# Performance work log

Hardware: AMD Instinct MI355X
Metric: run time of the kernel (lower is better)

Reference implementation:

```python
import jax, jax.numpy as jnp
import numpy as np

B, TT, T, L, V, E, H = 16, 8, 64, 100, 32000, 512, 512
EO = 2 * H          # encoder output size == decoder hidden size
A = 512             # attention size
IN = E + EO + E     # decoder raw input size
TEMP = IN // 2      # sharp_linear output size
sg = jax.lax.stop_gradient


def _lstm_cell(x, h, c, Wih, Whh, bih, bhh):
    # PyTorch LSTM gate order: i, f, g, o
    g = x @ Wih.T + bih + h @ Whh.T + bhh
    i, f, gg, o = jnp.split(g, 4, axis=-1)
    c = jax.nn.sigmoid(f) * c + jax.nn.sigmoid(i) * jnp.tanh(gg)
    h = jax.nn.sigmoid(o) * jnp.tanh(c)
    return h, c


def setup_inputs():
    key = jax.random.key(0)
    ks = jax.random.split(key, 24)
    s = 0.05
    rn = lambda k, sh: jax.random.normal(k, sh, jnp.float32) * s
    z = lambda *sh: jnp.zeros(sh, jnp.float32)
    return {
        "embedding": rn(ks[0], (V, E)),
        "enc_Wih_f": rn(ks[1], (4 * H, E)), "enc_Whh_f": rn(ks[2], (4 * H, H)),
        "enc_bih_f": z(4 * H), "enc_bhh_f": z(4 * H),
        "enc_Wih_b": rn(ks[3], (4 * H, E)), "enc_Whh_b": rn(ks[4], (4 * H, H)),
        "enc_bih_b": z(4 * H), "enc_bhh_b": z(4 * H),
        "W1": rn(ks[5], (A, EO)), "W2": rn(ks[6], (A, EO)),
        "mem_W": rn(ks[7], (E, EO)), "mem_b": z(E),
        "U1": rn(ks[8], (E, E)), "V1": rn(ks[9], (E, E)),
        "U2": rn(ks[10], (E, E)), "V2": rn(ks[11], (E, E)),
        "sharp_W": rn(ks[12], (TEMP, IN)), "sharp_b": z(TEMP),
        "dec_Wih": rn(ks[13], (4 * EO, TEMP)), "dec_Whh": rn(ks[14], (4 * EO, EO)),
        "dec_bih": z(4 * EO), "dec_bhh": z(4 * EO),
        "fc_W": rn(ks[15], (V, EO)), "fc_b": z(V),
        "topic": jax.random.randint(ks[16], (B, TT), 0, V),
        "topic_len": jnp.full((B,), TT, jnp.int32),
        "essay_input": jax.random.randint(ks[17], (B, T), 0, V),
        "essay_len": jnp.full((B,), T, jnp.int32),
        "mems": jax.random.randint(ks[18], (B, L), 0, V),
    }


def reference(embedding, enc_Wih_f, enc_Whh_f, enc_bih_f, enc_bhh_f,
              enc_Wih_b, enc_Whh_b, enc_bih_b, enc_bhh_b,
              W1, W2, mem_W, mem_b, U1, V1, U2, V2,
              sharp_W, sharp_b, dec_Wih, dec_Whh, dec_bih, dec_bhh,
              fc_W, fc_b, topic, topic_len, essay_input, essay_len, mems):
    Bsz = topic.shape[0]
    Tlen = essay_input.shape[1]

    # ---------------- Encoder (1-layer bidirectional LSTM) ----------------
    # all topic_len equal -> pack/sort is identity
    x = embedding[topic].transpose(1, 0, 2)  # [TT, B, E]

    def mk_cell(Wih, Whh, bih, bhh):
        def f(carry, xt):
            h, c = carry
            h, c = _lstm_cell(xt, h, c, Wih, Whh, bih, bhh)
            return (h, c), h
        return f

    z0 = (jnp.zeros((Bsz, H), x.dtype), jnp.zeros((Bsz, H), x.dtype))
    (hf, cf), outs_f = jax.lax.scan(mk_cell(enc_Wih_f, enc_Whh_f, enc_bih_f, enc_bhh_f), z0, x)
    (hb, cb), outs_b = jax.lax.scan(mk_cell(enc_Wih_b, enc_Whh_b, enc_bih_b, enc_bhh_b), z0, x[::-1])
    outs_b = outs_b[::-1]
    topics = jnp.concatenate([outs_f, outs_b], axis=-1).transpose(1, 0, 2)  # [B, TT, 2H]
    h = jnp.concatenate([hf, hb], axis=-1)  # [B, EO]
    c = jnp.concatenate([cf, cb], axis=-1)  # [B, EO]

    # ---------------- external memory ----------------
    M = embedding[mems]                      # [B, L, E]
    pre_t = topics @ W1.T                    # [B, TT, A]  (precompute attention keys)

    def update_memory(M, emb):
        # all reads of stored memory are detached in the original module
        Md = sg(M)
        e = emb[:, None, :]                  # [B, 1, E]
        Mt = jnp.tanh(Md @ U1.T + e @ V1.T)
        gate = jax.nn.sigmoid(Md @ U2.T + e @ V2.T)
        Mn = gate * Mt + (1.0 - gate) * Md
        return jnp.where(jnp.isfinite(Mn), Mn, jnp.float32(1e-31))

    def before_feed(emb, h_last, c_last, M):
        # topic attention (query = decoder cell state)
        q = c_last @ W2.T                                       # [B, A]
        alpha = jax.nn.softmax(jnp.einsum('bta,ba->bt', pre_t, q), axis=1)
        c_t = jnp.einsum('btd,bt->bd', topics, alpha)           # [B, EO]
        # content-addressed memory read (query = decoder hidden)
        v = jnp.tanh(h_last @ mem_W.T + mem_b)                  # [B, E]
        Md = sg(M)
        qm = jax.nn.softmax(jnp.einsum('ble,be->bl', Md, v), axis=1)
        m_t = jnp.einsum('bl,ble->be', qm, Md)                  # [B, E]
        return jnp.concatenate([emb, c_t, m_t], axis=1)         # [B, IN]

    # ---------------- decode (teacher forcing) ----------------
    emb0 = embedding[essay_input[:, 0]]
    M = update_memory(M, emb0)
    dec_in = before_feed(emb0, h, c, M)

    # steps 1..T-1 feed essay_input[:, t]; last scan step's memory update is unused
    toks = jnp.concatenate([essay_input[:, 1:], essay_input[:, -1:]], axis=1).T  # [T, B]

    def step(carry, tok):
        h, c, M, dec_in = carry
        xs = dec_in @ sharp_W.T + sharp_b
        h, c = _lstm_cell(xs, h, c, dec_Wih, dec_Whh, dec_bih, dec_bhh)
        logits = h @ fc_W.T + fc_b                              # [B, V]
        emb = embedding[tok]
        M = update_memory(M, emb)
        dec_in = before_feed(emb, h, c, M)
        return (h, c, M, dec_in), logits

    _, logits = jax.lax.scan(step, (h, c, M, dec_in), toks)
    return logits.transpose(1, 0, 2)  # [B, T, V]
```

## Files before the change

kernel.cpp:

```cpp
#include <hip/hip_runtime.h>
#include <math.h>

#define DEVI __device__ __forceinline__

typedef unsigned short us8 __attribute__((ext_vector_type(8)));
typedef short bfv __attribute__((ext_vector_type(8)));
typedef float f32x4 __attribute__((ext_vector_type(4)));

DEVI float sigmf_(float x){ return 1.0f/(1.0f+expf(-x)); }
DEVI float dot4_(const float4 a, const float4 b){ return a.x*b.x + a.y*b.y + a.z*b.z + a.w*b.w; }
DEVI float wred64(float v){
#pragma unroll
  for (int m = 32; m; m >>= 1) v += __shfl_xor(v, m);
  return v;
}
DEVI float b2f(unsigned short u){ return __uint_as_float(((unsigned)u)<<16); }
DEVI unsigned short f2bf(float x){
  unsigned u = __float_as_uint(x);
  return (unsigned short)((u + 0x7FFFu + ((u>>16)&1u)) >> 16);
}
DEVI void f2bf2(float x, unsigned short& hi, unsigned short& lo){
  hi = f2bf(x);
  lo = f2bf(x - b2f(hi));
}
DEVI unsigned short f2bf_lo(float x, unsigned short hi){
  return f2bf(x - b2f(hi));
}

DEVI float dotg(const unsigned short* wb, const float4* xr, int i8, float acc){
  us8 w = ((const us8*)wb)[i8];
  float4 xa = xr[2*i8], xb = xr[2*i8+1];
  acc += b2f(w[0])*xa.x; acc += b2f(w[1])*xa.y; acc += b2f(w[2])*xa.z; acc += b2f(w[3])*xa.w;
  acc += b2f(w[4])*xb.x; acc += b2f(w[5])*xb.y; acc += b2f(w[6])*xb.z; acc += b2f(w[7])*xb.w;
  return acc;
}
DEVI float dotg(const float* wb, const float4* xr, int i8, float acc){
  float4 wa = ((const float4*)wb)[2*i8], wv = ((const float4*)wb)[2*i8+1];
  float4 xa = xr[2*i8], xb = xr[2*i8+1];
  acc += wa.x*xa.x; acc += wa.y*xa.y; acc += wa.z*xa.z; acc += wa.w*xa.w;
  acc += wv.x*xb.x; acc += wv.y*xb.y; acc += wv.z*xb.z; acc += wv.w*xb.w;
  return acc;
}
template<typename WT>
DEVI float kdot1024(const WT* wbase, const float4* xr){
  float a0=0,a1=0,a2=0,a3=0;
#pragma unroll 4
  for (int it = 0; it < 32; ++it){
    a0 = dotg(wbase, xr, it*4+0, a0);
    a1 = dotg(wbase, xr, it*4+1, a1);
    a2 = dotg(wbase, xr, it*4+2, a2);
    a3 = dotg(wbase, xr, it*4+3, a3);
  }
  return (a0+a1)+(a2+a3);
}


__global__ void zero2_k(float* __restrict__ a, float* __restrict__ b, int n){
  int i = blockIdx.x*256 + threadIdx.x;
  if (i < n){ a[i] = 0.f; b[i] = 0.f; }
}

__global__ void gather_k(const float* __restrict__ emb, const int* __restrict__ topic,
                         const int* __restrict__ essay, const int* __restrict__ mems,
                         float* __restrict__ xtop, float* __restrict__ embs,
                         float* __restrict__ Mraw,
                         unsigned short* __restrict__ Mhi, unsigned short* __restrict__ Mlo)
{
  int r = blockIdx.x, tid = threadIdx.x;
  int idx; float* dst; size_t boff = 0; bool wb = false;
  if (r < 128){ int tt = r>>4, b = r&15; idx = topic[b*8+tt]; dst = xtop + (size_t)r*512; }
  else if (r < 1168){ int rr = r-128; int s = rr>>4, b = rr&15; int col = s < 64 ? s : 63;
                      idx = essay[b*64+col]; dst = embs + (size_t)rr*512; }
  else { int rr = r-1168; idx = mems[rr]; dst = Mraw + (size_t)rr*512;
         boff = (size_t)rr*512; wb = (Mhi != nullptr); }
  const float4* s4 = (const float4*)(emb + (size_t)idx*512);
  float4 v = s4[tid];
  ((float4*)dst)[tid] = v;
  if (wb){
    ushort4 h, l;
    f2bf2(v.x, h.x, l.x); f2bf2(v.y, h.y, l.y);
    f2bf2(v.z, h.z, l.z); f2bf2(v.w, h.w, l.w);
    ((ushort4*)(Mhi+boff))[tid] = h;
    ((ushort4*)(Mlo+boff))[tid] = l;
  }
}

__global__ void pack_k(const float* __restrict__ U1, const float* __restrict__ U2,
                       const float* __restrict__ sharpW,
                       float* __restrict__ UcatI, float* __restrict__ Ws3T)
{
  int gid = blockIdx.x*256 + threadIdx.x;
  if (gid < 524288){
    int n = gid>>9, k = gid&511;
    UcatI[gid] = (n&1) ? U2[(size_t)(n>>1)*512+k] : U1[(size_t)(n>>1)*512+k];
  } else {
    int g2 = gid - 524288;
    int k = g2>>10, j = g2&1023;
    Ws3T[g2] = sharpW[(size_t)j*2048 + 1536 + k];
  }
}

__global__ void pack_u_hilo(const float* __restrict__ U1, const float* __restrict__ U2,
                            unsigned short* __restrict__ Uhi, unsigned short* __restrict__ Ulo)
{
  int gid = blockIdx.x*256 + threadIdx.x;
  int n = gid>>9, k = gid&511;
  float v = (n&1) ? U2[(size_t)(n>>1)*512+k] : U1[(size_t)(n>>1)*512+k];
  unsigned short h, l;
  f2bf2(v, h, l);
  Uhi[gid] = h; Ulo[gid] = l;
}

__global__ void pack_ws3b(const float* __restrict__ sharpW,
                          unsigned short* __restrict__ hi, unsigned short* __restrict__ lo)
{
  int gid = blockIdx.x*256 + threadIdx.x;
  int j = gid>>9, k = gid&511;
  float v = sharpW[(size_t)j*2048 + 1536 + k];
  unsigned short h, l;
  f2bf2(v, h, l);
  hi[gid] = h; lo[gid] = l;
}

__global__ void conv_k(const float* __restrict__ src, unsigned short* __restrict__ dst, int n8){
  int i = blockIdx.x*256 + threadIdx.x;
  if (i >= n8) return;
  float4 a = ((const float4*)src)[2*i], b = ((const float4*)src)[2*i+1];
  us8 o;
  o[0]=f2bf(a.x); o[1]=f2bf(a.y); o[2]=f2bf(a.z); o[3]=f2bf(a.w);
  o[4]=f2bf(b.x); o[5]=f2bf(b.y); o[6]=f2bf(b.z); o[7]=f2bf(b.w);
  ((us8*)dst)[i] = o;
}

__global__ void conv2_k(const float* __restrict__ src,
                        unsigned short* __restrict__ hi, unsigned short* __restrict__ lo, int n8){
  int i = blockIdx.x*256 + threadIdx.x;
  if (i >= n8) return;
  float4 a = ((const float4*)src)[2*i], b = ((const float4*)src)[2*i+1];
  us8 oh, ol;
  oh[0]=f2bf(a.x); ol[0]=f2bf_lo(a.x, oh[0]);
  oh[1]=f2bf(a.y); ol[1]=f2bf_lo(a.y, oh[1]);
  oh[2]=f2bf(a.z); ol[2]=f2bf_lo(a.z, oh[2]);
  oh[3]=f2bf(a.w); ol[3]=f2bf_lo(a.w, oh[3]);
  oh[4]=f2bf(b.x); ol[4]=f2bf_lo(b.x, oh[4]);
  oh[5]=f2bf(b.y); ol[5]=f2bf_lo(b.y, oh[5]);
  oh[6]=f2bf(b.z); ol[6]=f2bf_lo(b.z, oh[6]);
  oh[7]=f2bf(b.w); ol[7]=f2bf_lo(b.w, oh[7]);
  ((us8*)hi)[i] = oh;
  ((us8*)lo)[i] = ol;
}

template<int ACT>
__global__ void gemm_nt(const float* __restrict__ A, int lda,
                        const float* __restrict__ W, int ldw, int woff,
                        const float* __restrict__ bias,
                        float* __restrict__ C, int ldc, int M, int N, int K)
{
  __shared__ float As[1024], Ws[1024];
  const int bm = blockIdx.y*64, bn = blockIdx.x*64;
  const int tid = threadIdx.x;
  const int lr = tid>>2, lk = (tid&3)<<2;
  const int tm = (tid>>4)<<2, tn = (tid&15)<<2;
  float acc[4][4] = {};
  for (int k0 = 0; k0 < K; k0 += 16){
    float4 av = make_float4(0.f,0.f,0.f,0.f);
    if (bm+lr < M) av = *(const float4*)(A + (size_t)(bm+lr)*lda + k0 + lk);
    As[(lk+0)*64+lr]=av.x; As[(lk+1)*64+lr]=av.y; As[(lk+2)*64+lr]=av.z; As[(lk+3)*64+lr]=av.w;
    float4 wv = make_float4(0.f,0.f,0.f,0.f);
    if (bn+lr < N) wv = *(const float4*)(W + (size_t)(bn+lr)*ldw + woff + k0 + lk);
    Ws[(lk+0)*64+lr]=wv.x; Ws[(lk+1)*64+lr]=wv.y; Ws[(lk+2)*64+lr]=wv.z; Ws[(lk+3)*64+lr]=wv.w;
    __syncthreads();
#pragma unroll
    for (int k = 0; k < 16; ++k){
      float4 a = *(const float4*)&As[k*64+tm];
      float4 w = *(const float4*)&Ws[k*64+tn];
      acc[0][0]+=a.x*w.x; acc[0][1]+=a.x*w.y; acc[0][2]+=a.x*w.z; acc[0][3]+=a.x*w.w;
      acc[1][0]+=a.y*w.x; acc[1][1]+=a.y*w.y; acc[1][2]+=a.y*w.z; acc[1][3]+=a.y*w.w;
      acc[2][0]+=a.z*w.x; acc[2][1]+=a.z*w.y; acc[2][2]+=a.z*w.z; acc[2][3]+=a.z*w.w;
      acc[3][0]+=a.w*w.x; acc[3][1]+=a.w*w.y; acc[3][2]+=a.w*w.z; acc[3][3]+=a.w*w.w;
    }
    __syncthreads();
  }
#pragma unroll
  for (int i = 0; i < 4; ++i){
    int m = bm+tm+i; if (m >= M) continue;
#pragma unroll
    for (int j = 0; j < 4; ++j){
      int n = bn+tn+j; if (n >= N) continue;
      float v = acc[i][j] + (bias ? bias[n] : 0.f);
      if (ACT == 1) v = tanhf(v);
      C[(size_t)m*ldc + n] = v;
    }
  }
}

__global__ void enc_step(const float* __restrict__ xtop,
    const float* __restrict__ Wih_f, const float* __restrict__ Whh_f,
    const float* __restrict__ bih_f, const float* __restrict__ bhh_f,
    const float* __restrict__ Wih_b, const float* __restrict__ Whh_b,
    const float* __restrict__ bih_b, const float* __restrict__ bhh_b,
    const float* __restrict__ h_in, const float* __restrict__ c_in,
    float* __restrict__ h_out, float* __restrict__ c_out,
    float* __restrict__ topics, int t)
{
  const int dir = blockIdx.y;
  const int j = blockIdx.x*4 + (threadIdx.x>>6);
  const int lane = threadIdx.x & 63;
  const int b = lane & 15, g4 = lane >> 4;
  const int tt = dir ? (7 - t) : t;
  const float* Wih = dir ? Wih_b : Wih_f;
  const float* Whh = dir ? Whh_b : Whh_f;
  const float* bih = dir ? bih_b : bih_f;
  const float* bhh = dir ? bhh_b : bhh_f;
  const int row = g4*512 + j;
  float acc = bih[row] + bhh[row];
  const float4* wx = (const float4*)(Wih + (size_t)row*512);
  const float4* xv = (const float4*)(xtop + (size_t)(tt*16+b)*512);
#pragma unroll 8
  for (int k = 0; k < 128; ++k) acc += dot4_(wx[k], xv[k]);
  const float4* wh = (const float4*)(Whh + (size_t)row*512);
  const float4* hv = (const float4*)(h_in + (size_t)b*1024 + dir*512);
#pragma unroll 8
  for (int k = 0; k < 128; ++k) acc += dot4_(wh[k], hv[k]);
  float gi = __shfl(acc, b);
  float gf = __shfl(acc, b+16);
  float gg = __shfl(acc, b+32);
  float go = __shfl(acc, b+48);
  if (g4 == 0){
    float c_old = c_in[(size_t)b*1024 + dir*512 + j];
    float cn = sigmf_(gf)*c_old + sigmf_(gi)*tanhf(gg);
    float hn = sigmf_(go)*tanhf(cn);
    h_out[(size_t)b*1024 + dir*512 + j] = hn;
    c_out[(size_t)b*1024 + dir*512 + j] = cn;
    topics[(size_t)(b*8+tt)*1024 + dir*512 + j] = hn;
  }
}

DEVI void mem_gemm_role(int bid, const float* __restrict__ Min, float* __restrict__ Mout,
                        const float* __restrict__ U,
                        const float* __restrict__ eV1s, const float* __restrict__ eV2s,
                        float* lds, int tid)
{
  const int bm = (bid>>4)*64, bn = (bid&15)*64;
  float* As = lds; float* Ws = lds + 1024;
  const int lr = tid>>2, lk = (tid&3)<<2;
  const int tm = (tid>>4)<<2, tn = (tid&15)<<2;
  float acc[4][4] = {};
  for (int k0 = 0; k0 < 512; k0 += 16){
    float4 av = *(const float4*)(Min + (size_t)(bm+lr)*512 + k0 + lk);
    As[(lk+0)*64+lr]=av.x; As[(lk+1)*64+lr]=av.y; As[(lk+2)*64+lr]=av.z; As[(lk+3)*64+lr]=av.w;
    float4 wv = *(const float4*)(U + (size_t)(bn+lr)*512 + k0 + lk);
    Ws[(lk+0)*64+lr]=wv.x; Ws[(lk+1)*64+lr]=wv.y; Ws[(lk+2)*64+lr]=wv.z; Ws[(lk+3)*64+lr]=wv.w;
    __syncthreads();
#pragma unroll
    for (int k = 0; k < 16; ++k){
      float4 a = *(const float4*)&As[k*64+tm];
      float4 w = *(const float4*)&Ws[k*64+tn];
      acc[0][0]+=a.x*w.x; acc[0][1]+=a.x*w.y; acc[0][2]+=a.x*w.z; acc[0][3]+=a.x*w.w;
      acc[1][0]+=a.y*w.x; acc[1][1]+=a.y*w.y; acc[1][2]+=a.y*w.z; acc[1][3]+=a.y*w.w;
      acc[2][0]+=a.z*w.x; acc[2][1]+=a.z*w.y; acc[2][2]+=a.z*w.z; acc[2][3]+=a.z*w.w;
      acc[3][0]+=a.w*w.x; acc[3][1]+=a.w*w.y; acc[3][2]+=a.w*w.z; acc[3][3]+=a.w*w.w;
    }
    __syncthreads();
  }
  const int e0 = (bn+tn)>>1;
#pragma unroll
  for (int i = 0; i < 4; ++i){
    int r = bm+tm+i;
    int b = r/100;
#pragma unroll
    for (int p = 0; p < 2; ++p){
      int e = e0 + p;
      float oldv = Min[(size_t)r*512 + e];
      float mt = tanhf (acc[i][2*p]   + eV1s[(size_t)b*512 + e]);
      float g  = sigmf_(acc[i][2*p+1] + eV2s[(size_t)b*512 + e]);
      float mn = g*mt + (1.f-g)*oldv;
      if (!isfinite(mn)) mn = 1e-31f;
      Mout[(size_t)r*512 + e] = mn;
    }
  }
}

__global__ void mem_update_k(const float* __restrict__ Min, float* __restrict__ Mout,
                             const float* __restrict__ U,
                             const float* __restrict__ eV1s, const float* __restrict__ eV2s)
{
  __shared__ float lds[2080];
  mem_gemm_role(blockIdx.x, Min, Mout, U, eV1s, eV2s, lds, threadIdx.x);
}

DEVI void mem_ep(f32x4 v, int m0, int n0, int i, int j, int kg, int r16, int lane,
                 const float* __restrict__ Min,
                 const float* __restrict__ eV1s, const float* __restrict__ eV2s,
                 float* __restrict__ Mout,
                 unsigned short* __restrict__ Mohi, unsigned short* __restrict__ Molo)
{
#pragma unroll
  for (int q = 0; q < 4; ++q){
    float val = v[q];
    float oth = __shfl_xor(val, 1);
    if (!(lane&1)){
      int m = m0 + i*16 + kg*4 + q;
      int n = n0 + j*16 + r16;
      int e = n>>1, bb = m/100;
      float mold = Min[(size_t)m*512 + e];
      float mt = tanhf (val + eV1s[(size_t)bb*512 + e]);
      float g  = sigmf_(oth + eV2s[(size_t)bb*512 + e]);
      float mn = g*mt + (1.f-g)*mold;
      if (!isfinite(mn)) mn = 1e-31f;
      Mout[(size_t)m*512 + e] = mn;
      unsigned short h, l;
      f2bf2(mn, h, l);
      Mohi[(size_t)m*512 + e] = h;
      Molo[(size_t)m*512 + e] = l;
    }
  }
}

DEVI void mem_mfma_role2(int hwbid, const float* __restrict__ Min,
                        const unsigned short* __restrict__ Mhi, const unsigned short* __restrict__ Mlo,
                        float* __restrict__ Mout,
                        unsigned short* __restrict__ Mohi, unsigned short* __restrict__ Molo,
                        const unsigned short* __restrict__ Uhi, const unsigned short* __restrict__ Ulo,
                        const float* __restrict__ eV1s, const float* __restrict__ eV2s,
                        int tid, float* __restrict__ lds)
{
  const int bid2 = (hwbid & 7)*200 + (hwbid >> 3);
  const int bm = (bid2 >> 5)*32, bn = (bid2 & 31)*32;
  const int wave = tid>>6, lane = tid&63;
  const int r16 = lane&15, kg = lane>>4;
  const size_t aoff = (size_t)(bm + r16)*512 + wave*128 + kg*8;
  const size_t boff = (size_t)(bn + r16)*512 + wave*128 + kg*8;
  const unsigned short* pa0h = Mhi + aoff; const unsigned short* pa0l = Mlo + aoff;
  const unsigned short* pb0h = Uhi + boff; const unsigned short* pb0l = Ulo + boff;
  f32x4 c00 = {}, c01 = {}, c10 = {}, c11 = {};
#pragma unroll
  for (int k0 = 0; k0 < 128; k0 += 32){
    bfv a0h = *(const bfv*)(pa0h + k0);
    bfv a0l = *(const bfv*)(pa0l + k0);
    bfv a1h = *(const bfv*)(pa0h + 16*512 + k0);
    bfv a1l = *(const bfv*)(pa0l + 16*512 + k0);
    bfv b0h = *(const bfv*)(pb0h + k0);
    bfv b0l = *(const bfv*)(pb0l + k0);
    bfv b1h = *(const bfv*)(pb0h + 16*512 + k0);
    bfv b1l = *(const bfv*)(pb0l + 16*512 + k0);
    c00 = __builtin_amdgcn_mfma_f32_16x16x32_bf16(a0h, b0h, c00, 0, 0, 0);
    c00 = __builtin_amdgcn_mfma_f32_16x16x32_bf16(a0h, b0l, c00, 0, 0, 0);
    c00 = __builtin_amdgcn_mfma_f32_16x16x32_bf16(a0l, b0h, c00, 0, 0, 0);
    c01 = __builtin_amdgcn_mfma_f32_16x16x32_bf16(a0h, b1h, c01, 0, 0, 0);
    c01 = __builtin_amdgcn_mfma_f32_16x16x32_bf16(a0h, b1l, c01, 0, 0, 0);
    c01 = __builtin_amdgcn_mfma_f32_16x16x32_bf16(a0l, b1h, c01, 0, 0, 0);
    c10 = __builtin_amdgcn_mfma_f32_16x16x32_bf16(a1h, b0h, c10, 0, 0, 0);
    c10 = __builtin_amdgcn_mfma_f32_16x16x32_bf16(a1h, b0l, c10, 0, 0, 0);
    c10 = __builtin_amdgcn_mfma_f32_16x16x32_bf16(a1l, b0h, c10, 0, 0, 0);
    c11 = __builtin_amdgcn_mfma_f32_16x16x32_bf16(a1h, b1h, c11, 0, 0, 0);
    c11 = __builtin_amdgcn_mfma_f32_16x16x32_bf16(a1h, b1l, c11, 0, 0, 0);
    c11 = __builtin_amdgcn_mfma_f32_16x16x32_bf16(a1l, b1h, c11, 0, 0, 0);
  }
  float* wbase = lds + wave*1024 + lane*4;
#pragma unroll
  for (int q = 0; q < 4; ++q){
    wbase[q]     = c00[q];
    wbase[256+q] = c01[q];
    wbase[512+q] = c10[q];
    wbase[768+q] = c11[q];
  }
  __syncthreads();
  f32x4 s;
#pragma unroll
  for (int q = 0; q < 4; ++q)
    s[q] = lds[       wave*256 + lane*4 + q] + lds[1024 + wave*256 + lane*4 + q]
         + lds[2048 + wave*256 + lane*4 + q] + lds[3072 + wave*256 + lane*4 + q];
  mem_ep(s, bm, bn, wave>>1, wave&1, kg, r16, lane, Min, eV1s, eV2s, Mout, Mohi, Molo);
}

__global__ __launch_bounds__(256,4) void mem_update_k2(
    const float* __restrict__ Min,
    const unsigned short* __restrict__ Mhi, const unsigned short* __restrict__ Mlo,
    float* __restrict__ Mout,
    unsigned short* __restrict__ Mohi, unsigned short* __restrict__ Molo,
    const unsigned short* __restrict__ Uhi, const unsigned short* __restrict__ Ulo,
    const float* __restrict__ eV1s, const float* __restrict__ eV2s)
{
  __shared__ float lds[4096];
  mem_mfma_role2(blockIdx.x, Min, Mhi, Mlo, Mout, Mohi, Molo, Uhi, Ulo, eV1s, eV2s, threadIdx.x, lds);
}

DEVI void logits_role(int lb, int tid,
    const unsigned short* __restrict__ fcWb, const float* __restrict__ fcb,
    const unsigned short* __restrict__ hh, const unsigned short* __restrict__ hl,
    float* __restrict__ out, int t)
{
  const int wave = tid>>6, lane = tid&63;
  const int r16 = lane&15, kg = lane>>4;
  const int tile = lb*4 + wave;
  const unsigned short* pa0 = fcWb + (size_t)(tile*16 + r16)*1024 + kg*8;
  const unsigned short* pbh = hh + (size_t)r16*1024 + kg*8;
  const unsigned short* pbl = hl + (size_t)r16*1024 + kg*8;
  f32x4 c0 = {};
#pragma unroll 4
  for (int k0 = 0; k0 < 1024; k0 += 32){
    bfv a0 = *(const bfv*)(pa0 + k0);
    bfv b0 = *(const bfv*)(pbh + k0);
    bfv b1 = *(const bfv*)(pbl + k0);
    c0 = __builtin_amdgcn_mfma_f32_16x16x32_bf16(a0, b0, c0, 0,0,0);
    c0 = __builtin_amdgcn_mfma_f32_16x16x32_bf16(a0, b1, c0, 0,0,0);
  }
  float* ob = out + (size_t)r16*2048000 + (size_t)t*32000;
#pragma unroll
  for (int q = 0; q < 4; ++q){
    int j0 = tile*16 + kg*4 + q;
    ob[j0] = c0[q] + fcb[j0];
  }
}

__global__ __launch_bounds__(256) void logits_k(
    const unsigned short* __restrict__ fcWb, const float* __restrict__ fcb,
    const unsigned short* __restrict__ hh, const unsigned short* __restrict__ hl,
    float* __restrict__ out, int t)
{
  logits_role(blockIdx.x, threadIdx.x, fcWb, fcb, hh, hl, out, t);
}

__global__ void step_pre(const float* __restrict__ Min, float* __restrict__ Mout,
    const float* __restrict__ U,
    const float* __restrict__ eV1s, const float* __restrict__ eV2s,
    const float* __restrict__ qb, const float* __restrict__ vb,
    const float* __restrict__ pret, const float* __restrict__ tws2,
    const float* __restrict__ eWs1t, const float* __restrict__ sharp_b,
    const float* __restrict__ Ws3T, float* __restrict__ xs)
{
  __shared__ float lds[2080];
  const int tid = threadIdx.x;
  if (blockIdx.x >= 16){
    mem_gemm_role(blockIdx.x-16, Min, Mout, U, eV1s, eV2s, lds, tid);
    return;
  }
  const int b = blockIdx.x;
  lds[tid]         = qb[b*512 + tid];
  lds[tid+256]     = qb[b*512 + tid + 256];
  lds[512+tid]     = vb[b*512 + tid];
  lds[512+tid+256] = vb[b*512 + tid + 256];
  __syncthreads();
  {
    const int tq = tid>>5, l32 = tid&31;
    const float* pr = pret + (size_t)(b*8+tq)*512;
    float sv = 0.f;
#pragma unroll
    for (int i = 0; i < 16; ++i){ int a = l32 + 32*i; sv += pr[a]*lds[a]; }
#pragma unroll
    for (int m = 16; m; m >>= 1) sv += __shfl_xor(sv, m);
    if (l32 == 0) lds[1024+tq] = sv;
  }
  __syncthreads();
  {
    float mx = -1e30f;
#pragma unroll
    for (int i = 0; i < 8; ++i) mx = fmaxf(mx, lds[1024+i]);
    float sm = 0.f; float ev[8];
#pragma unroll
    for (int i = 0; i < 8; ++i){ ev[i] = expf(lds[1024+i]-mx); sm += ev[i]; }
    if (tid < 8) lds[1032+tid] = ev[tid]/sm;
  }
  __syncthreads();
  {
    const int wv = tid>>6, lane = tid&63;
    for (int l = wv; l < 100; l += 4){
      const float* Mr = Min + (size_t)(b*100+l)*512;
      float sv = 0.f;
#pragma unroll
      for (int i = 0; i < 8; ++i){ int k = lane + 64*i; sv += Mr[k]*lds[512+k]; }
      sv = wred64(sv);
      if (lane == 0) lds[1040+l] = sv;
    }
  }
  __syncthreads();
  float mx = -1e30f;
  for (int i = 0; i < 100; ++i) mx = fmaxf(mx, lds[1040+i]);
  __syncthreads();
  if (tid < 100) lds[1040+tid] = expf(lds[1040+tid]-mx);
  __syncthreads();
  float sm = 0.f;
  for (int i = 0; i < 100; ++i) sm += lds[1040+i];
  const float inv = 1.f/sm;
  for (int e = tid; e < 512; e += 256){
    float a = 0.f;
    for (int l = 0; l < 100; ++l) a += lds[1040+l]*Min[(size_t)(b*100+l)*512 + e];
    lds[1152+e] = a*inv;
  }
  __syncthreads();
  float a0[4];
#pragma unroll
  for (int r2 = 0; r2 < 4; ++r2){
    int j = tid + 256*r2;
    float v = sharp_b[j] + eWs1t[(size_t)b*1024 + j];
#pragma unroll
    for (int t2 = 0; t2 < 8; ++t2) v += lds[1032+t2]*tws2[(size_t)(b*8+t2)*1024 + j];
    a0[r2] = v;
  }
  for (int k = 0; k < 512; ++k){
    float mk = lds[1152+k];
    const float* wr = Ws3T + (size_t)k*1024;
    a0[0] += mk*wr[tid];
    a0[1] += mk*wr[tid+256];
    a0[2] += mk*wr[tid+512];
    a0[3] += mk*wr[tid+768];
  }
#pragma unroll
  for (int r2 = 0; r2 < 4; ++r2) xs[(size_t)b*1024 + tid + 256*r2] = a0[r2];
}

__global__ __launch_bounds__(256,4) void attn_mega(
    const float* __restrict__ Min,
    const unsigned short* __restrict__ Mhi, const unsigned short* __restrict__ Mlo,
    float* __restrict__ Mout,
    unsigned short* __restrict__ Mohi, unsigned short* __restrict__ Molo,
    const unsigned short* __restrict__ Uhi, const unsigned short* __restrict__ Ulo,
    const float* __restrict__ eV1s, const float* __restrict__ eV2s,
    const float* __restrict__ qb, const float* __restrict__ vb,
    const float* __restrict__ pret,
    float* __restrict__ alphab,
    unsigned short* __restrict__ mthi, unsigned short* __restrict__ mtlo,
    const unsigned short* __restrict__ fcWb, const float* __restrict__ fcb,
    const unsigned short* __restrict__ hph, const unsigned short* __restrict__ hpl,
    float* __restrict__ out, int tlog, int nLog)
{
  __shared__ float lds[4096];
  const int tid = threadIdx.x;
  if (blockIdx.x >= 128){
    const int bid = blockIdx.x - 128;
    if (bid < nLog){
      logits_role(bid, tid, fcWb, fcb, hph, hpl, out, tlog);
      return;
    }
    mem_mfma_role2(bid - nLog, Min, Mhi, Mlo, Mout, Mohi, Molo, Uhi, Ulo, eV1s, eV2s, tid, lds);
    return;
  }
  const int b = blockIdx.x >> 3, ec = blockIdx.x & 7;
  lds[tid]         = qb[b*512 + tid];
  lds[tid+256]     = qb[b*512 + tid + 256];
  lds[512+tid]     = vb[b*512 + tid];
  lds[512+tid+256] = vb[b*512 + tid + 256];
  __syncthreads();
  if (ec == 0){
    {
      const int tq = tid>>5, l32 = tid&31;
      const float* pr = pret + (size_t)(b*8+tq)*512;
      float sv = 0.f;
#pragma unroll
      for (int i = 0; i < 16; ++i){ int a = l32 + 32*i; sv += pr[a]*lds[a]; }
#pragma unroll
      for (int m = 16; m; m >>= 1) sv += __shfl_xor(sv, m);
      if (l32 == 0) lds[1024+tq] = sv;
    }
    __syncthreads();
    {
      float mx = -1e30f;
#pragma unroll
      for (int i = 0; i < 8; ++i) mx = fmaxf(mx, lds[1024+i]);
      float sm = 0.f; float ev[8];
#pragma unroll
      for (int i = 0; i < 8; ++i){ ev[i] = expf(lds[1024+i]-mx); sm += ev[i]; }
      if (tid < 8) alphab[b*8+tid] = ev[tid]/sm;
    }
    __syncthreads();
  }
  {
    const int wv = tid>>6, lane = tid&63;
    for (int l = wv; l < 100; l += 4){
      const float* Mr = Min + (size_t)(b*100+l)*512;
      float sv = 0.f;
#pragma unroll
      for (int i = 0; i < 8; ++i){ int k = lane + 64*i; sv += Mr[k]*lds[512+k]; }
      sv = wred64(sv);
      if (lane == 0) lds[1040+l] = sv;
    }
  }
  __syncthreads();
  {
    const int wv = tid>>6;
    float v100 = (tid < 100) ? lds[1040+tid] : -1e30f;
    float m1 = v100;
#pragma unroll
    for (int m = 32; m; m >>= 1) m1 = fmaxf(m1, __shfl_xor(m1, m));
    if ((tid&63) == 0) lds[1664+wv] = m1;
    __syncthreads();
    float mx = fmaxf(fmaxf(lds[1664], lds[1665]), fmaxf(lds[1666], lds[1667]));
    float e = (tid < 100) ? expf(v100 - mx) : 0.f;
    float s1 = e;
#pragma unroll
    for (int m = 32; m; m >>= 1) s1 += __shfl_xor(s1, m);
    if ((tid&63) == 0) lds[1668+wv] = s1;
    __syncthreads();
    float sm = lds[1668]+lds[1669]+lds[1670]+lds[1671];
    if (tid < 100) lds[1800+tid] = e/sm;
  }
  __syncthreads();
  {
    const int e = ec*64 + (tid & 63);
    const int lg = tid >> 6;
    float a = 0.f;
    for (int l = lg*25; l < lg*25 + 25; ++l)
      a += lds[1800+l] * Min[(size_t)(b*100 + l)*512 + e];
    lds[1904 + lg*64 + (tid & 63)] = a;
    __syncthreads();
    if (lg == 0){
      float s = lds[1904 + tid] + lds[1968 + tid] + lds[2032 + tid] + lds[2096 + tid];
      unsigned short h, l2;
      f2bf2(s, h, l2);
      mthi[b*512 + e] = h;
      mtlo[b*512 + e] = l2;
    }
  }
}

__global__ __launch_bounds__(256) void xs_k(
    const unsigned short* __restrict__ Ws3hi, const unsigned short* __restrict__ Ws3lo,
    const unsigned short* __restrict__ mthi, const unsigned short* __restrict__ mtlo,
    const float* __restrict__ alphab, const float* __restrict__ sharp_b,
    const float* __restrict__ eWs1t, const float* __restrict__ tws2,
    unsigned short* __restrict__ xshi, unsigned short* __restrict__ xslo)
{
  __shared__ float lds[1024];
  const int tid = threadIdx.x, wave = tid>>6, lane = tid&63;
  const int r16 = lane&15, kg = lane>>4;
  const int jt = blockIdx.x;
  const size_t aoff = (size_t)(jt*16 + r16)*512 + wave*128 + kg*8;
  const size_t boff = (size_t)r16*512 + wave*128 + kg*8;
  f32x4 c0 = {};
#pragma unroll
  for (int k0 = 0; k0 < 128; k0 += 32){
    bfv ah = *(const bfv*)(Ws3hi + aoff + k0);
    bfv al = *(const bfv*)(Ws3lo + aoff + k0);
    bfv bh = *(const bfv*)(mthi + boff + k0);
    bfv bl = *(const bfv*)(mtlo + boff + k0);
    c0 = __builtin_amdgcn_mfma_f32_16x16x32_bf16(ah, bh, c0, 0,0,0);
    c0 = __builtin_amdgcn_mfma_f32_16x16x32_bf16(ah, bl, c0, 0,0,0);
    c0 = __builtin_amdgcn_mfma_f32_16x16x32_bf16(al, bh, c0, 0,0,0);
  }
  float* wb2 = lds + wave*256 + lane*4;
#pragma unroll
  for (int q = 0; q < 4; ++q) wb2[q] = c0[q];
  __syncthreads();
  if (wave == 0){
    const int b = r16;
#pragma unroll
    for (int q = 0; q < 4; ++q){
      float s = lds[lane*4+q] + lds[256+lane*4+q] + lds[512+lane*4+q] + lds[768+lane*4+q];
      int j = jt*16 + kg*4 + q;
      float v2 = s + sharp_b[j] + eWs1t[(size_t)b*1024 + j];
#pragma unroll
      for (int t2 = 0; t2 < 8; ++t2) v2 += alphab[b*8+t2]*tws2[(size_t)(b*8+t2)*1024 + j];
      unsigned short h, l;
      f2bf2(v2, h, l);
      xshi[b*1024+j] = h;
      xslo[b*1024+j] = l;
    }
  }
}

__global__ void dec_lstm(const float* __restrict__ xs,
    const float* __restrict__ Wih, const float* __restrict__ Whh,
    const float* __restrict__ bih, const float* __restrict__ bhh,
    const float* __restrict__ h_in, const float* __restrict__ c_in,
    float* __restrict__ h_out, float* __restrict__ c_out)
{
  const int j = blockIdx.x*4 + (threadIdx.x>>6);
  const int lane = threadIdx.x & 63;
  const int b = lane & 15, g4 = lane >> 4;
  const int row = g4*1024 + j;
  float acc = bih[row] + bhh[row];
  const float4* w1 = (const float4*)(Wih + (size_t)row*1024);
  const float4* x1 = (const float4*)(xs + (size_t)b*1024);
#pragma unroll 8
  for (int k = 0; k < 256; ++k) acc += dot4_(w1[k], x1[k]);
  const float4* w2 = (const float4*)(Whh + (size_t)row*1024);
  const float4* h1 = (const float4*)(h_in + (size_t)b*1024);
#pragma unroll 8
  for (int k = 0; k < 256; ++k) acc += dot4_(w2[k], h1[k]);
  float gi = __shfl(acc, b);
  float gf = __shfl(acc, b+16);
  float gg = __shfl(acc, b+32);
  float go = __shfl(acc, b+48);
  if (g4 == 0){
    float c_old = c_in[(size_t)b*1024 + j];
    float cn = sigmf_(gf)*c_old + sigmf_(gi)*tanhf(gg);
    float hn = sigmf_(go)*tanhf(cn);
    h_out[(size_t)b*1024 + j] = hn;
    c_out[(size_t)b*1024 + j] = cn;
  }
}

__global__ __launch_bounds__(256) void dec_mfma(
    const unsigned short* __restrict__ xsh, const unsigned short* __restrict__ xsl,
    const unsigned short* __restrict__ Wih_h, const unsigned short* __restrict__ Wih_l,
    const unsigned short* __restrict__ Whh_h, const unsigned short* __restrict__ Whh_l,
    const float* __restrict__ bih, const float* __restrict__ bhh,
    const unsigned short* __restrict__ hih, const unsigned short* __restrict__ hil,
    const float* __restrict__ c_in,
    float* __restrict__ h_out, float* __restrict__ c_out,
    unsigned short* __restrict__ hoh, unsigned short* __restrict__ hol,
    unsigned short* __restrict__ coh, unsigned short* __restrict__ col_)
{
  __shared__ float acc_lds[4][4][64][4];
  __shared__ float gat[4][64][4];
  const int tid = threadIdx.x, kh = tid>>6, lane = tid&63;
  const int r16 = lane&15, kg = lane>>4;
  const int jt = blockIdx.x;
  const size_t arow = (size_t)(jt*16 + r16)*1024 + kh*256 + kg*8;
  const size_t boff = (size_t)r16*1024 + kh*256 + kg*8;
  f32x4 c0 = {}, c1 = {}, c2 = {}, c3 = {};
#pragma unroll 2
  for (int k0 = 0; k0 < 256; k0 += 32){
    bfv bxh = *(const bfv*)(xsh + boff + k0);
    bfv bxl = *(const bfv*)(xsl + boff + k0);
    bfv bhh_ = *(const bfv*)(hih + boff + k0);
    bfv bhl_ = *(const bfv*)(hil + boff + k0);
#define DEC_GATE(G, CC) { \
    bfv aih = *(const bfv*)(Wih_h + arow + (size_t)(G)*1048576 + k0); \
    bfv ail = *(const bfv*)(Wih_l + arow + (size_t)(G)*1048576 + k0); \
    bfv ahh = *(const bfv*)(Whh_h + arow + (size_t)(G)*1048576 + k0); \
    bfv ahl = *(const bfv*)(Whh_l + arow + (size_t)(G)*1048576 + k0); \
    CC = __builtin_amdgcn_mfma_f32_16x16x32_bf16(aih, bxh, CC, 0,0,0); \
    CC = __builtin_amdgcn_mfma_f32_16x16x32_bf16(aih, bxl, CC, 0,0,0); \
    CC = __builtin_amdgcn_mfma_f32_16x16x32_bf16(ail, bxh, CC, 0,0,0); \
    CC = __builtin_amdgcn_mfma_f32_16x16x32_bf16(ahh, bhh_, CC, 0,0,0); \
    CC = __builtin_amdgcn_mfma_f32_16x16x32_bf16(ahh, bhl_, CC, 0,0,0); \
    CC = __builtin_amdgcn_mfma_f32_16x16x32_bf16(ahl, bhh_, CC, 0,0,0); }
    DEC_GATE(0, c0)
    DEC_GATE(1, c1)
    DEC_GATE(2, c2)
    DEC_GATE(3, c3)
#undef DEC_GATE
  }
#pragma unroll
  for (int q = 0; q < 4; ++q){
    acc_lds[kh][0][lane][q] = c0[q];
    acc_lds[kh][1][lane][q] = c1[q];
    acc_lds[kh][2][lane][q] = c2[q];
    acc_lds[kh][3][lane][q] = c3[q];
  }
  __syncthreads();
  {
    const int g = kh;
#pragma unroll
    for (int q = 0; q < 4; ++q)
      gat[g][lane][q] = acc_lds[0][g][lane][q] + acc_lds[1][g][lane][q]
                      + acc_lds[2][g][lane][q] + acc_lds[3][g][lane][q];
  }
  __syncthreads();
  {
    const int b = tid&15, joff = tid>>4;
    const int l2 = (joff>>2)*16 + b, q2 = joff&3;
    const int j = jt*16 + joff;
    float gi = gat[0][l2][q2] + bih[j]        + bhh[j];
    float gf = gat[1][l2][q2] + bih[1024+j]   + bhh[1024+j];
    float gg = gat[2][l2][q2] + bih[2048+j]   + bhh[2048+j];
    float go = gat[3][l2][q2] + bih[3072+j]   + bhh[3072+j];
    float cold = c_in[b*1024 + j];
    float cn = sigmf_(gf)*cold + sigmf_(gi)*tanhf(gg);
    float hn = sigmf_(go)*tanhf(cn);
    h_out[b*1024 + j] = hn;
    c_out[b*1024 + j] = cn;
    unsigned short uh, ul;
    f2bf2(hn, uh, ul); hoh[b*1024+j] = uh; hol[b*1024+j] = ul;
    f2bf2(cn, uh, ul); coh[b*1024+j] = uh; col_[b*1024+j] = ul;
  }
}

__global__ __launch_bounds__(256) void qv_k(
    const unsigned short* __restrict__ W2h, const unsigned short* __restrict__ W2l,
    const unsigned short* __restrict__ mWh, const unsigned short* __restrict__ mWl,
    const float* __restrict__ memb,
    const unsigned short* __restrict__ hh, const unsigned short* __restrict__ hl,
    const unsigned short* __restrict__ ch, const unsigned short* __restrict__ cl,
    float* __restrict__ qb, float* __restrict__ vb)
{
  __shared__ float lds[1024];
  const int tid = threadIdx.x, wave = tid>>6, lane = tid&63;
  const int r16 = lane&15, kg = lane>>4;
  const bool isV = blockIdx.x >= 32;
  const int tile = isV ? ((int)blockIdx.x - 32) : (int)blockIdx.x;
  const unsigned short* Ah = isV ? mWh : W2h;
  const unsigned short* Al = isV ? mWl : W2l;
  const unsigned short* Bh = isV ? hh : ch;
  const unsigned short* Bl = isV ? hl : cl;
  const size_t aoff = (size_t)(tile*16 + r16)*1024 + wave*256 + kg*8;
  const size_t boff = (size_t)r16*1024 + wave*256 + kg*8;
  f32x4 c0 = {};
#pragma unroll
  for (int k0 = 0; k0 < 256; k0 += 32){
    bfv ah = *(const bfv*)(Ah + aoff + k0);
    bfv al = *(const bfv*)(Al + aoff + k0);
    bfv b0 = *(const bfv*)(Bh + boff + k0);
    bfv b1 = *(const bfv*)(Bl + boff + k0);
    c0 = __builtin_amdgcn_mfma_f32_16x16x32_bf16(ah, b0, c0, 0,0,0);
    c0 = __builtin_amdgcn_mfma_f32_16x16x32_bf16(ah, b1, c0, 0,0,0);
    c0 = __builtin_amdgcn_mfma_f32_16x16x32_bf16(al, b0, c0, 0,0,0);
  }
  float* wb2 = lds + wave*256 + lane*4;
#pragma unroll
  for (int q = 0; q < 4; ++q) wb2[q] = c0[q];
  __syncthreads();
  if (wave == 0){
#pragma unroll
    for (int q = 0; q < 4; ++q){
      float s = lds[lane*4+q] + lds[256+lane*4+q] + lds[512+lane*4+q] + lds[768+lane*4+q];
      int j = tile*16 + kg*4 + q;
      if (isV) vb[r16*512 + j] = tanhf(s + memb[j]);
      else     qb[r16*512 + j] = s;
    }
  }
}

template<typename WT>
__global__ __launch_bounds__(256,4) void step_out_t(const float* __restrict__ h, const float* __restrict__ c,
    const WT* __restrict__ fcW_, const float* __restrict__ fcb,
    const float* __restrict__ W2, const float* __restrict__ memW,
    const float* __restrict__ memb,
    float* __restrict__ out, float* __restrict__ qb, float* __restrict__ vb, int t)
{
  __shared__ float tile[256];
  const int bid = blockIdx.x;
  const int wv = threadIdx.x>>6, lane = threadIdx.x&63;
  const int b = lane&15, jj = lane>>4;
  if (bid < 2000){
    const int j = bid*16 + wv*4 + jj;
    float acc = kdot1024(fcW_ + (size_t)j*1024, (const float4*)(h + (size_t)b*1024));
    tile[(wv*4+jj)*16 + b] = acc;
    __syncthreads();
    const int b2 = threadIdx.x>>4, j2 = threadIdx.x&15;
    out[(size_t)b2*2048000 + (size_t)t*32000 + bid*16 + j2] = tile[j2*16+b2] + fcb[bid*16+j2];
  } else if (bid < 2032){
    const int j = (bid-2000)*16 + wv*4 + jj;
    float acc = kdot1024(W2 + (size_t)j*1024, (const float4*)(c + (size_t)b*1024));
    qb[b*512 + j] = acc;
  } else {
    const int j = (bid-2032)*16 + wv*4 + jj;
    float acc = kdot1024(memW + (size_t)j*1024, (const float4*)(h + (size_t)b*1024));
    vb[b*512 + j] = tanhf(acc + memb[j]);
  }
}

extern "C" void kernel_launch(void* const* d_in, const int* in_sizes, int n_in,
                              void* d_out, int out_size, void* d_ws, size_t ws_size,
                              hipStream_t stream)
{
  const float* embedding = (const float*)d_in[0];
  const float* Wih_f = (const float*)d_in[1];
  const float* Whh_f = (const float*)d_in[2];
  const float* bih_f = (const float*)d_in[3];
  const float* bhh_f = (const float*)d_in[4];
  const float* Wih_b = (const float*)d_in[5];
  const float* Whh_b = (const float*)d_in[6];
  const float* bih_b = (const float*)d_in[7];
  const float* bhh_b = (const float*)d_in[8];
  const float* W1    = (const float*)d_in[9];
  const float* W2    = (const float*)d_in[10];
  const float* mem_W = (const float*)d_in[11];
  const float* mem_b = (const float*)d_in[12];
  const float* U1    = (const float*)d_in[13];
  const float* V1    = (const float*)d_in[14];
  const float* U2    = (const float*)d_in[15];
  const float* V2    = (const float*)d_in[16];
  const float* sharp_W = (const float*)d_in[17];
  const float* sharp_b = (const float*)d_in[18];
  const float* dec_Wih = (const float*)d_in[19];
  const float* dec_Whh = (const float*)d_in[20];
  const float* dec_bih = (const float*)d_in[21];
  const float* dec_bhh = (const float*)d_in[22];
  const float* fc_W  = (const float*)d_in[23];
  const float* fc_b  = (const float*)d_in[24];
  const int* topic   = (const int*)d_in[25];
  const int* essay   = (const int*)d_in[27];
  const int* mems    = (const int*)d_in[29];
  float* out = (float*)d_out;
  float* ws = (float*)d_ws;

  float* x_topic = ws;
  float* embs    = ws + 65536;
  float* eV1     = ws + 598016;
  float* eV2     = ws + 1130496;
  float* eWs1    = ws + 1662976;
  float* topics  = ws + 2727936;
  float* tws2    = ws + 2859008;
  float* pret    = ws + 2990080;
  float* Mb0     = ws + 3055616;
  float* Mb1     = ws + 3874816;
  float* h_buf   = ws + 4694016;
  float* c_buf   = ws + 4726784;
  float* xs      = ws + 4759552;
  float* qb      = ws + 4775936;
  float* vb      = ws + 4784128;
  float* UcatI   = ws + 4792320;
  float* Ws3T    = ws + 5316608;
  unsigned short* Ws3hi = (unsigned short*)(ws + 4792320);
  unsigned short* Ws3lo = (unsigned short*)(ws + 5054464);
  unsigned short* mthi  = (unsigned short*)(ws + 5316608);
  unsigned short* mtlo  = (unsigned short*)(ws + 5320704);
  float*          alphab= ws + 5324800;
  unsigned short* Uhi   = (unsigned short*)(ws + 5840896);
  unsigned short* Ulo   = (unsigned short*)(ws + 6103040);
  unsigned short* Mb0hi = (unsigned short*)(ws + 6365184);
  unsigned short* Mb0lo = (unsigned short*)(ws + 6774784);
  unsigned short* Mb1hi = (unsigned short*)(ws + 7184384);
  unsigned short* Mb1lo = (unsigned short*)(ws + 7593984);
  unsigned short* fcWb  = (unsigned short*)(ws + 8003584);
  unsigned short* dWihHi = (unsigned short*)(ws + 24387584);
  unsigned short* dWihLo = (unsigned short*)(ws + 26484736);
  unsigned short* dWhhHi = (unsigned short*)(ws + 28581888);
  unsigned short* dWhhLo = (unsigned short*)(ws + 30679040);
  unsigned short* W2h    = (unsigned short*)(ws + 32776192);
  unsigned short* W2l    = (unsigned short*)(ws + 33038336);
  unsigned short* mWh    = (unsigned short*)(ws + 33300480);
  unsigned short* mWl    = (unsigned short*)(ws + 33562624);
  unsigned short* hbhi   = (unsigned short*)(ws + 33824768);
  unsigned short* hblo   = (unsigned short*)(ws + 33841152);
  unsigned short* cbhi   = (unsigned short*)(ws + 33857536);
  unsigned short* cblo   = (unsigned short*)(ws + 33873920);
  unsigned short* xshi   = (unsigned short*)(ws + 33890304);
  unsigned short* xslo   = (unsigned short*)(ws + 33898496);

  const size_t NEED2 = (size_t)24387584 * 4;
  const size_t NEED3 = (size_t)33906688 * 4;
  const int tier = (ws_size >= NEED3) ? 3 : (ws_size >= NEED2 ? 2 : 0);

  if (tier < 3){
    zero2_k<<<64,256,0,stream>>>(h_buf, c_buf, 16384);
    gather_k<<<2768,128,0,stream>>>(embedding, topic, essay, mems, x_topic, embs, Mb1, nullptr, nullptr);
    pack_k<<<4096,256,0,stream>>>(U1, U2, sharp_W, UcatI, Ws3T);
    if (tier == 2) conv_k<<<16000,256,0,stream>>>(fc_W, fcWb, 4096000);
    gemm_nt<0><<<dim3(8,17),256,0,stream>>>(embs,512, V1,512,0, nullptr, eV1,512, 1040,512,512);
    gemm_nt<0><<<dim3(8,17),256,0,stream>>>(embs,512, V2,512,0, nullptr, eV2,512, 1040,512,512);
    gemm_nt<0><<<dim3(16,17),256,0,stream>>>(embs,512, sharp_W,2048,0, nullptr, eWs1,1024, 1040,1024,512);
    for (int t = 0; t < 8; ++t){
      const float* hi = h_buf + (t&1)*16384;
      const float* ci = c_buf + (t&1)*16384;
      float* ho = h_buf + ((t+1)&1)*16384;
      float* co = c_buf + ((t+1)&1)*16384;
      enc_step<<<dim3(128,2),256,0,stream>>>(x_topic, Wih_f,Whh_f,bih_f,bhh_f,
                                             Wih_b,Whh_b,bih_b,bhh_b, hi,ci,ho,co, topics, t);
    }
    gemm_nt<0><<<dim3(8,2),256,0,stream>>>(topics,1024, W1,1024,0, nullptr, pret,512, 128,512,1024);
    gemm_nt<0><<<dim3(16,2),256,0,stream>>>(topics,1024, sharp_W,2048,512, nullptr, tws2,1024, 128,1024,1024);
    gemm_nt<0><<<dim3(8,1),256,0,stream>>>(c_buf,1024, W2,1024,0, nullptr, qb,512, 16,512,1024);
    gemm_nt<1><<<dim3(8,1),256,0,stream>>>(h_buf,1024, mem_W,1024,0, mem_b, vb,512, 16,512,1024);
    mem_update_k<<<400,256,0,stream>>>(Mb1, Mb0, UcatI, eV1, eV2);
    for (int t = 0; t < 64; ++t){
      float* Mi = (t&1) ? Mb1 : Mb0;
      float* Mo = (t&1) ? Mb0 : Mb1;
      int nb = (t < 63) ? 416 : 16;
      step_pre<<<nb,256,0,stream>>>(Mi, Mo, UcatI,
          eV1 + (size_t)(t+1)*8192, eV2 + (size_t)(t+1)*8192,
          qb, vb, pret, tws2, eWs1 + (size_t)t*16384, sharp_b, Ws3T, xs);
      const float* hi = h_buf + (t&1)*16384;
      const float* ci = c_buf + (t&1)*16384;
      float* ho = h_buf + ((t+1)&1)*16384;
      float* co = c_buf + ((t+1)&1)*16384;
      dec_lstm<<<256,256,0,stream>>>(xs, dec_Wih, dec_Whh, dec_bih, dec_bhh, hi, ci, ho, co);
      if (tier == 2)
        step_out_t<unsigned short><<<2064,256,0,stream>>>(ho, co, fcWb, fc_b, W2, mem_W, mem_b, out, qb, vb, t);
      else
        step_out_t<float><<<2064,256,0,stream>>>(ho, co, fc_W, fc_b, W2, mem_W, mem_b, out, qb, vb, t);
    }
    return;
  }

  zero2_k<<<64,256,0,stream>>>(h_buf, c_buf, 16384);
  gather_k<<<2768,128,0,stream>>>(embedding, topic, essay, mems, x_topic, embs, Mb1, Mb1hi, Mb1lo);
  pack_u_hilo<<<2048,256,0,stream>>>(U1, U2, Uhi, Ulo);
  pack_ws3b<<<2048,256,0,stream>>>(sharp_W, Ws3hi, Ws3lo);
  conv_k<<<16000,256,0,stream>>>(fc_W, fcWb, 4096000);
  conv2_k<<<2048,256,0,stream>>>(dec_Wih, dWihHi, dWihLo, 524288);
  conv2_k<<<2048,256,0,stream>>>(dec_Whh, dWhhHi, dWhhLo, 524288);
  conv2_k<<<256,256,0,stream>>>(W2, W2h, W2l, 65536);
  conv2_k<<<256,256,0,stream>>>(mem_W, mWh, mWl, 65536);

  gemm_nt<0><<<dim3(8,17),256,0,stream>>>(embs,512, V1,512,0, nullptr, eV1,512, 1040,512,512);
  gemm_nt<0><<<dim3(8,17),256,0,stream>>>(embs,512, V2,512,0, nullptr, eV2,512, 1040,512,512);
  gemm_nt<0><<<dim3(16,17),256,0,stream>>>(embs,512, sharp_W,2048,0, nullptr, eWs1,1024, 1040,1024,512);

  for (int t = 0; t < 8; ++t){
    const float* hi = h_buf + (t&1)*16384;
    const float* ci = c_buf + (t&1)*16384;
    float* ho = h_buf + ((t+1)&1)*16384;
    float* co = c_buf + ((t+1)&1)*16384;
    enc_step<<<dim3(128,2),256,0,stream>>>(x_topic, Wih_f,Whh_f,bih_f,bhh_f,
                                           Wih_b,Whh_b,bih_b,bhh_b, hi,ci,ho,co, topics, t);
  }
  gemm_nt<0><<<dim3(8,2),256,0,stream>>>(topics,1024, W1,1024,0, nullptr, pret,512, 128,512,1024);
  gemm_nt<0><<<dim3(16,2),256,0,stream>>>(topics,1024, sharp_W,2048,512, nullptr, tws2,1024, 128,1024,1024);
  gemm_nt<0><<<dim3(8,1),256,0,stream>>>(c_buf,1024, W2,1024,0, nullptr, qb,512, 16,512,1024);
  gemm_nt<1><<<dim3(8,1),256,0,stream>>>(h_buf,1024, mem_W,1024,0, mem_b, vb,512, 16,512,1024);
  conv2_k<<<8,256,0,stream>>>(h_buf, hbhi, hblo, 2048);
  conv2_k<<<8,256,0,stream>>>(c_buf, cbhi, cblo, 2048);
  mem_update_k2<<<1600,256,0,stream>>>(Mb1, Mb1hi, Mb1lo, Mb0, Mb0hi, Mb0lo, Uhi, Ulo, eV1, eV2);

  for (int t = 0; t < 64; ++t){
    float* Mi = (t&1) ? Mb1 : Mb0;
    unsigned short* Mihi = (t&1) ? Mb1hi : Mb0hi;
    unsigned short* Milo = (t&1) ? Mb1lo : Mb0lo;
    float* Mo = (t&1) ? Mb0 : Mb1;
    unsigned short* Mohi = (t&1) ? Mb0hi : Mb1hi;
    unsigned short* Molo = (t&1) ? Mb0lo : Mb1lo;
    const int par = t&1, nxt = (t+1)&1;
    const int nLog = (t > 0) ? 500 : 0;
    const int nGemm = (t < 63) ? 1600 : 0;
    attn_mega<<<128 + nLog + nGemm,256,0,stream>>>(Mi, Mihi, Milo, Mo, Mohi, Molo, Uhi, Ulo,
        eV1 + (size_t)(t+1)*8192, eV2 + (size_t)(t+1)*8192,
        qb, vb, pret, alphab, mthi, mtlo,
        fcWb, fc_b, hbhi + par*16384, hblo + par*16384, out, t-1, nLog);
    xs_k<<<64,256,0,stream>>>(Ws3hi, Ws3lo, mthi, mtlo, alphab, sharp_b,
        eWs1 + (size_t)t*16384, tws2, xshi, xslo);
    const float* ci = c_buf + par*16384;
    float* ho = h_buf + nxt*16384;
    float* co = c_buf + nxt*16384;
    dec_mfma<<<64,256,0,stream>>>(xshi, xslo, dWihHi, dWihLo, dWhhHi, dWhhLo,
        dec_bih, dec_bhh,
        hbhi + par*16384, hblo + par*16384, ci,
        ho, co,
        hbhi + nxt*16384, hblo + nxt*16384, cbhi + nxt*16384, cblo + nxt*16384);
    if (t < 63)
      qv_k<<<64,256,0,stream>>>(W2h, W2l, mWh, mWl, mem_b,
          hbhi + nxt*16384, hblo + nxt*16384, cbhi + nxt*16384, cblo + nxt*16384, qb, vb);
  }
  logits_k<<<500,256,0,stream>>>(fcWb, fc_b, hbhi, hblo, out, 63);
}
```

Before: 6.817 ms.

## Split decoder LSTM gates across blocks with last-block-wins reduction

The decoder LSTM MFMA kernel now launches one block per (row tile, gate) pair instead of one per row tile, quadrupling the grid to spread the weight streaming over more CUs. Each block writes partial gate sums to a global scratch buffer, and an atomic counter picks the last-arriving block of each tile to reduce the partials and apply the cell nonlinearity. This trades an LDS reduction for global memory traffic, threadfences and atomics, and relies on the counter being reset correctly each step.

```diff
diff --git a/kernel.cpp b/kernel.cpp
--- a/kernel.cpp
+++ b/kernel.cpp
@@ -691,7 +691,7 @@
   }
 }
 
-__global__ __launch_bounds__(256) void dec_mfma(
+__global__ __launch_bounds__(256) void dec_mfma2(
     const unsigned short* __restrict__ xsh, const unsigned short* __restrict__ xsl,
     const unsigned short* __restrict__ Wih_h, const unsigned short* __restrict__ Wih_l,
     const unsigned short* __restrict__ Whh_h, const unsigned short* __restrict__ Whh_l,
@@ -700,63 +700,58 @@
     const float* __restrict__ c_in,
     float* __restrict__ h_out, float* __restrict__ c_out,
     unsigned short* __restrict__ hoh, unsigned short* __restrict__ hol,
-    unsigned short* __restrict__ coh, unsigned short* __restrict__ col_)
-{
-  __shared__ float acc_lds[4][4][64][4];
-  __shared__ float gat[4][64][4];
+    unsigned short* __restrict__ coh, unsigned short* __restrict__ col_,
+    float* __restrict__ pgat, int* __restrict__ cnt)
+{
+  __shared__ int winflag;
   const int tid = threadIdx.x, kh = tid>>6, lane = tid&63;
   const int r16 = lane&15, kg = lane>>4;
-  const int jt = blockIdx.x;
-  const size_t arow = (size_t)(jt*16 + r16)*1024 + kh*256 + kg*8;
+  const int jt = blockIdx.x>>2, g = blockIdx.x&3;
+  const size_t arow = (size_t)(jt*16 + r16)*1024 + kh*256 + kg*8 + (size_t)g*1048576;
   const size_t boff = (size_t)r16*1024 + kh*256 + kg*8;
-  f32x4 c0 = {}, c1 = {}, c2 = {}, c3 = {};
+  f32x4 cc = {};
 #pragma unroll 2
   for (int k0 = 0; k0 < 256; k0 += 32){
     bfv bxh = *(const bfv*)(xsh + boff + k0);
     bfv bxl = *(const bfv*)(xsl + boff + k0);
     bfv bhh_ = *(const bfv*)(hih + boff + k0);
     bfv bhl_ = *(const bfv*)(hil + boff + k0);
-#define DEC_GATE(G, CC) { \
-    bfv aih = *(const bfv*)(Wih_h + arow + (size_t)(G)*1048576 + k0); \
-    bfv ail = *(const bfv*)(Wih_l + arow + (size_t)(G)*1048576 + k0); \
-    bfv ahh = *(const bfv*)(Whh_h + arow + (size_t)(G)*1048576 + k0); \
-    bfv ahl = *(const bfv*)(Whh_l + arow + (size_t)(G)*1048576 + k0); \
-    CC = __builtin_amdgcn_mfma_f32_16x16x32_bf16(aih, bxh, CC, 0,0,0); \
-    CC = __builtin_amdgcn_mfma_f32_16x16x32_bf16(aih, bxl, CC, 0,0,0); \
-    CC = __builtin_amdgcn_mfma_f32_16x16x32_bf16(ail, bxh, CC, 0,0,0); \
-    CC = __builtin_amdgcn_mfma_f32_16x16x32_bf16(ahh, bhh_, CC, 0,0,0); \
-    CC = __builtin_amdgcn_mfma_f32_16x16x32_bf16(ahh, bhl_, CC, 0,0,0); \
-    CC = __builtin_amdgcn_mfma_f32_16x16x32_bf16(ahl, bhh_, CC, 0,0,0); }
-    DEC_GATE(0, c0)
-    DEC_GATE(1, c1)
-    DEC_GATE(2, c2)
-    DEC_GATE(3, c3)
-#undef DEC_GATE
-  }
-#pragma unroll
-  for (int q = 0; q < 4; ++q){
-    acc_lds[kh][0][lane][q] = c0[q];
-    acc_lds[kh][1][lane][q] = c1[q];
-    acc_lds[kh][2][lane][q] = c2[q];
-    acc_lds[kh][3][lane][q] = c3[q];
-  }
-  __syncthreads();
-  {
-    const int g = kh;
-#pragma unroll
-    for (int q = 0; q < 4; ++q)
-      gat[g][lane][q] = acc_lds[0][g][lane][q] + acc_lds[1][g][lane][q]
-                      + acc_lds[2][g][lane][q] + acc_lds[3][g][lane][q];
-  }
-  __syncthreads();
-  {
+    bfv aih = *(const bfv*)(Wih_h + arow + k0);
+    bfv ail = *(const bfv*)(Wih_l + arow + k0);
+    bfv ahh = *(const bfv*)(Whh_h + arow + k0);
+    bfv ahl = *(const bfv*)(Whh_l + arow + k0);
+    cc = __builtin_amdgcn_mfma_f32_16x16x32_bf16(aih, bxh, cc, 0,0,0);
+    cc = __builtin_amdgcn_mfma_f32_16x16x32_bf16(aih, bxl, cc, 0,0,0);
+    cc = __builtin_amdgcn_mfma_f32_16x16x32_bf16(ail, bxh, cc, 0,0,0);
+    cc = __builtin_amdgcn_mfma_f32_16x16x32_bf16(ahh, bhh_, cc, 0,0,0);
+    cc = __builtin_amdgcn_mfma_f32_16x16x32_bf16(ahh, bhl_, cc, 0,0,0);
+    cc = __builtin_amdgcn_mfma_f32_16x16x32_bf16(ahl, bhh_, cc, 0,0,0);
+  }
+  float* pg = pgat + ((((size_t)jt*4 + g)*4 + kh)*256);
+#pragma unroll
+  for (int q = 0; q < 4; ++q) pg[(kg*4+q)*16 + r16] = cc[q];
+  __threadfence();
+  __syncthreads();
+  if (tid == 0){
+    int old = atomicAdd(cnt + jt, 1);
+    winflag = (old == 3) ? 1 : 0;
+  }
+  __syncthreads();
+  if (winflag){
+    __threadfence();
     const int b = tid&15, joff = tid>>4;
-    const int l2 = (joff>>2)*16 + b, q2 = joff&3;
     const int j = jt*16 + joff;
-    float gi = gat[0][l2][q2] + bih[j]        + bhh[j];
-    float gf = gat[1][l2][q2] + bih[1024+j]   + bhh[1024+j];
-    float gg = gat[2][l2][q2] + bih[2048+j]   + bhh[2048+j];
-    float go = gat[3][l2][q2] + bih[3072+j]   + bhh[3072+j];
+    const float* pj = pgat + (size_t)jt*4096;
+    float gv[4];
+#pragma unroll
+    for (int g2 = 0; g2 < 4; ++g2){
+      gv[g2] = pj[(g2*4+0)*256 + joff*16 + b] + pj[(g2*4+1)*256 + joff*16 + b]
+             + pj[(g2*4+2)*256 + joff*16 + b] + pj[(g2*4+3)*256 + joff*16 + b];
+    }
+    float gi = gv[0] + bih[j]        + bhh[j];
+    float gf = gv[1] + bih[1024+j]   + bhh[1024+j];
+    float gg = gv[2] + bih[2048+j]   + bhh[2048+j];
+    float go = gv[3] + bih[3072+j]   + bhh[3072+j];
     float cold = c_in[b*1024 + j];
     float cn = sigmf_(gf)*cold + sigmf_(gi)*tanhf(gg);
     float hn = sigmf_(go)*tanhf(cn);
@@ -765,6 +760,7 @@
     unsigned short uh, ul;
     f2bf2(hn, uh, ul); hoh[b*1024+j] = uh; hol[b*1024+j] = ul;
     f2bf2(cn, uh, ul); coh[b*1024+j] = uh; col_[b*1024+j] = ul;
+    if (tid == 0) cnt[jt] = 0;
   }
 }
 
@@ -899,6 +895,8 @@
   unsigned short* mthi  = (unsigned short*)(ws + 5316608);
   unsigned short* mtlo  = (unsigned short*)(ws + 5320704);
   float*          alphab= ws + 5324800;
+  float*          pgat  = ws + 5324928;
+  int*            cnt   = (int*)(ws + 5587072);
   unsigned short* Uhi   = (unsigned short*)(ws + 5840896);
   unsigned short* Ulo   = (unsigned short*)(ws + 6103040);
   unsigned short* Mb0hi = (unsigned short*)(ws + 6365184);
@@ -967,6 +965,7 @@
   }
 
   zero2_k<<<64,256,0,stream>>>(h_buf, c_buf, 16384);
+  hipMemsetAsync(cnt, 0, 64*sizeof(int), stream);
   gather_k<<<2768,128,0,stream>>>(embedding, topic, essay, mems, x_topic, embs, Mb1, Mb1hi, Mb1lo);
   pack_u_hilo<<<2048,256,0,stream>>>(U1, U2, Uhi, Ulo);
   pack_ws3b<<<2048,256,0,stream>>>(sharp_W, Ws3hi, Ws3lo);
@@ -1015,11 +1014,12 @@
     const float* ci = c_buf + par*16384;
     float* ho = h_buf + nxt*16384;
     float* co = c_buf + nxt*16384;
-    dec_mfma<<<64,256,0,stream>>>(xshi, xslo, dWihHi, dWihLo, dWhhHi, dWhhLo,
+    dec_mfma2<<<256,256,0,stream>>>(xshi, xslo, dWihHi, dWihLo, dWhhHi, dWhhLo,
         dec_bih, dec_bhh,
         hbhi + par*16384, hblo + par*16384, ci,
         ho, co,
-        hbhi + nxt*16384, hblo + nxt*16384, cbhi + nxt*16384, cblo + nxt*16384);
+        hbhi + nxt*16384, hblo + nxt*16384, cbhi + nxt*16384, cblo + nxt*16384,
+        pgat, cnt);
     if (t < 63)
       qv_k<<<64,256,0,stream>>>(W2h, W2l, mWh, mWl, mem_b,
           hbhi + nxt*16384, hblo + nxt*16384, cbhi + nxt*16384, cblo + nxt*16384, qb, vb);
```

After: 8.681 ms. 27.3% more time.
